# Kernel tuning notes

Measured on AMD Instinct MI355X. Metric: run time of the kernel, lower is better.

Reference implementation:

```python
import jax, jax.numpy as jnp
import numpy as np

LORA_ALPHA = 32
RANK = 16
TOP_K = 2
SCALING = LORA_ALPHA / RANK  # lora_alpha / r
EPS = 1e-9


def setup_inputs() -> dict:
    key = jax.random.key(0)
    ks = jax.random.split(key, 6)
    B, S, D_IN, D_OUT, E, R = 4, 2048, 4096, 4096, 8, RANK
    x = jax.random.normal(ks[0], (B, S, D_IN), dtype=jnp.float32)
    W = jax.random.normal(ks[1], (D_OUT, D_IN), dtype=jnp.float32) * (1.0 / np.sqrt(D_IN))
    bias = jax.random.normal(ks[2], (D_OUT,), dtype=jnp.float32) * 0.02
    route_W = jax.random.normal(ks[3], (E, D_IN), dtype=jnp.float32) * (1.0 / np.sqrt(D_IN))
    lora_A = jax.random.normal(ks[4], (E, R, D_IN), dtype=jnp.float32) * (1.0 / np.sqrt(D_IN))
    lora_B = jax.random.normal(ks[5], (D_OUT, R), dtype=jnp.float32)
    lora_B = jnp.broadcast_to(lora_B, (E, D_OUT, R)) * 0.01  # small nonzero so lora path matters
    return {"x": x, "W": W, "bias": bias, "route_W": route_W,
            "lora_A": lora_A, "lora_B": jnp.asarray(lora_B)}


def reference(x, W, bias, route_W, lora_A, lora_B):
    # Base dense projection: y = x W^T + b   [B,S,out]
    base = jnp.einsum('bsi,oi->bso', x, W) + bias

    # Router: softmax over experts in fp32, then top-k gating
    gate_score = jnp.einsum('bsi,ei->bse', x, route_W)          # [B,S,E]
    probs = jax.nn.softmax(gate_score.astype(jnp.float32), axis=-1)
    topk_vals, topk_idx = jax.lax.top_k(probs, TOP_K)           # [B,S,k]
    # renorm (top_k < lora_nums)
    topk_vals = topk_vals / (jnp.sum(topk_vals, axis=-1, keepdims=True) + EPS)
    # dense routing weights: zeros with top-k values scattered back  [B,S,E]
    E = probs.shape[-1]
    routing_weight = jnp.sum(
        jax.nn.one_hot(topk_idx, E, dtype=base.dtype) * topk_vals[..., None].astype(base.dtype),
        axis=-2)

    # Expert LoRA: identical math to the gather/index_add loop, expressed as
    # a dense weighted combine (weights are exactly 0 for unrouted experts).
    xf = x.astype(jnp.float32)
    h = jnp.einsum('bsi,eri->bser', xf, lora_A.astype(jnp.float32))      # [B,S,E,r] (small)
    hw = h * routing_weight.astype(jnp.float32)[..., None]               # gate per expert
    lora_out = jnp.einsum('bser,eor->bso', hw, lora_B.astype(jnp.float32))

    result = base + lora_out.astype(base.dtype) * SCALING
    return result, routing_weight, gate_score
```

## Files before the change

### kernel.cpp

```cpp
#include <hip/hip_runtime.h>
#include <hip/hip_bf16.h>

typedef __bf16 bf16_t;
typedef __bf16 bf16x8 __attribute__((ext_vector_type(8)));
typedef float floatx4 __attribute__((ext_vector_type(4)));

#define M_TOK 8192
#define K_DIM 4096
#define N_OUT 4096
#define NEXP  8
#define LRANK 16
#define KEXT  128
#define SCALING 2.0f

#define GLOAD_LDS16(g, l) \
    __builtin_amdgcn_global_load_lds((const __attribute__((address_space(1))) void*)(g), \
                                     (__attribute__((address_space(3))) void*)(l), 16, 0, 0)


__device__ __forceinline__ void pack4(bf16_t* dst, float4 v) {
    union { bf16_t h[4]; uint2 u; } t;
    t.h[0] = (bf16_t)v.x; t.h[1] = (bf16_t)v.y;
    t.h[2] = (bf16_t)v.z; t.h[3] = (bf16_t)v.w;
    *(uint2*)dst = t.u;
}

__device__ __forceinline__ void cvt8_body(const float* __restrict__ src,
                                          bf16_t* __restrict__ dst, int blk) {
    size_t i = (size_t)blk * 256 + threadIdx.x;
    float4 a = ((const float4*)src)[i * 2];
    float4 b = ((const float4*)src)[i * 2 + 1];
    union { bf16_t h[8]; uint4 u; } t;
    t.h[0] = (bf16_t)a.x; t.h[1] = (bf16_t)a.y; t.h[2] = (bf16_t)a.z; t.h[3] = (bf16_t)a.w;
    t.h[4] = (bf16_t)b.x; t.h[5] = (bf16_t)b.y; t.h[6] = (bf16_t)b.z; t.h[7] = (bf16_t)b.w;
    ((uint4*)dst)[i] = t.u;
}


#define PREP_W_BLKS   8192
#define PREP_A_BLKS   256
#define PREP_B_BLKS   2048

__global__ __launch_bounds__(256) void prep_all(const float* __restrict__ W,
                                                const float* __restrict__ loraA,
                                                const float* __restrict__ loraB,
                                                bf16_t* __restrict__ Wb,
                                                bf16_t* __restrict__ aflat,
                                                bf16_t* __restrict__ bflat) {
    int b = blockIdx.x;
    if (b < PREP_W_BLKS) {
        cvt8_body(W, Wb, b);
    } else if (b < PREP_W_BLKS + PREP_A_BLKS) {
        cvt8_body(loraA, aflat, b - PREP_W_BLKS);
    } else {
        int g = (b - PREP_W_BLKS - PREP_A_BLKS) * 256 + threadIdx.x;
        int o = g >> 7, j = g & 127;
        int e = j >> 4, r = j & 15;
        bflat[g] = (bf16_t)loraB[((size_t)e * N_OUT + o) * LRANK + r];
    }
}


__global__ __launch_bounds__(256) void gate_cvt16(const float* __restrict__ x,
                                                  const float* __restrict__ routeW,
                                                  bf16_t* __restrict__ xb,
                                                  float* __restrict__ rw_out,
                                                  float* __restrict__ gate_out)
{
    __shared__ float rwT[NEXP][256];
    int tid = threadIdx.x, lane = tid & 63, wave = tid >> 6;
    int tl = lane >> 4, seg = lane & 15;
    int t = blockIdx.x * 16 + wave * 4 + tl;
    const float* xrow = x + (size_t)t * K_DIM;
    bf16_t* xbrow = xb + (size_t)t * K_DIM;

    float acc[NEXP];
    #pragma unroll
    for (int e = 0; e < NEXP; ++e) acc[e] = 0.f;

    int srow = tid >> 5, scol = (tid & 31) * 8;

    for (int kk = 0; kk < K_DIM / 256; ++kk) {
        {
            const float4* src = (const float4*)(routeW + (size_t)srow * K_DIM + kk * 256 + scol);
            float4 v0 = src[0], v1 = src[1];
            *(float4*)&rwT[srow][scol]     = v0;
            *(float4*)&rwT[srow][scol + 4] = v1;
        }
        __syncthreads();
        #pragma unroll
        for (int kc = 0; kc < 4; ++kc) {
            int kloc = kc * 64 + seg * 4;
            int k = kk * 256 + kloc;
            float4 xv = *(const float4*)(xrow + k);
            union { bf16_t h[4]; uint2 u; } cv;
            cv.h[0] = (bf16_t)xv.x; cv.h[1] = (bf16_t)xv.y;
            cv.h[2] = (bf16_t)xv.z; cv.h[3] = (bf16_t)xv.w;
            *(uint2*)(xbrow + k) = cv.u;
            #pragma unroll
            for (int e = 0; e < NEXP; ++e) {
                float4 wv = *(const float4*)&rwT[e][kloc];
                acc[e] += xv.x * wv.x + xv.y * wv.y + xv.z * wv.z + xv.w * wv.w;
            }
        }
        __syncthreads();
    }

    #pragma unroll
    for (int e = 0; e < NEXP; ++e) {
        acc[e] += __shfl_xor(acc[e], 1);
        acc[e] += __shfl_xor(acc[e], 2);
        acc[e] += __shfl_xor(acc[e], 4);
        acc[e] += __shfl_xor(acc[e], 8);
    }

    if (seg == 0) {
        float mx = acc[0];
        #pragma unroll
        for (int e = 1; e < NEXP; ++e) mx = fmaxf(mx, acc[e]);
        float p[NEXP], s = 0.f;
        #pragma unroll
        for (int e = 0; e < NEXP; ++e) { p[e] = expf(acc[e] - mx); s += p[e]; }
        float inv_s = 1.0f / s;
        #pragma unroll
        for (int e = 0; e < NEXP; ++e) p[e] *= inv_s;
        int i0 = 0;
        #pragma unroll
        for (int e = 1; e < NEXP; ++e) if (p[e] > p[i0]) i0 = e;
        int i1 = (i0 == 0) ? 1 : 0;
        #pragma unroll
        for (int e = 0; e < NEXP; ++e) { if (e == i0 || e == i1) continue; if (p[e] > p[i1]) i1 = e; }
        float v0 = p[i0], v1 = p[i1];
        float inv = 1.0f / (v0 + v1 + 1e-9f);
        float r[NEXP];
        #pragma unroll
        for (int e = 0; e < NEXP; ++e) r[e] = 0.f;
        r[i0] = v0 * inv; r[i1] = v1 * inv;
        #pragma unroll
        for (int e = 0; e < NEXP; ++e) {
            gate_out[(size_t)t * NEXP + e] = acc[e];
            rw_out[(size_t)t * NEXP + e]  = r[e];
        }
    }
}


__global__ __launch_bounds__(256) void h_kernel_v3(const bf16_t* __restrict__ xb,
                                                   const bf16_t* __restrict__ aflat,
                                                   const float* __restrict__ rw,
                                                   bf16_t* __restrict__ hw)
{
    __shared__ bf16_t As[4 * 32 * 32];
    __shared__ bf16_t Bs[4 * 128 * 32];
    int tid = threadIdx.x, lane = tid & 63, wave = tid >> 6;
    int lrow = lane & 15, lq = lane >> 4;
    int n0 = wave * 32;
    int m0 = blockIdx.x * 32;
    floatx4 acc[2][2] = {};

    const bf16_t* srcA[2];
    #pragma unroll
    for (int i = 0; i < 2; ++i) {
        int idx = i * 256 + tid;
        int ks = idx >> 7, r = (idx >> 2) & 31, cc2 = idx & 3;
        srcA[i] = xb + (size_t)(m0 + r) * K_DIM + ks * 32 + cc2 * 8;
    }
    const bf16_t* srcB[8];
    #pragma unroll
    for (int i = 0; i < 8; ++i) {
        int idx = i * 256 + tid;
        int ks = idx >> 9, r = (idx >> 2) & 127, cc2 = idx & 3;
        srcB[i] = aflat + (size_t)r * K_DIM + ks * 32 + cc2 * 8;
    }

    for (int k0 = 0; k0 < K_DIM; k0 += 128) {
        #pragma unroll
        for (int i = 0; i < 2; ++i)
            GLOAD_LDS16(srcA[i] + k0, (char*)As + (i * 256 + wave * 64) * 16);
        #pragma unroll
        for (int i = 0; i < 8; ++i)
            GLOAD_LDS16(srcB[i] + k0, (char*)Bs + (i * 256 + wave * 64) * 16);
        __syncthreads();
        #pragma unroll
        for (int ks = 0; ks < 4; ++ks) {
            bf16x8 af[2], bfr[2];
            #pragma unroll
            for (int mi = 0; mi < 2; ++mi)
                af[mi] = *(const bf16x8*)(As + ks * 1024 + (mi * 16 + lrow) * 32 + lq * 8);
            #pragma unroll
            for (int ni = 0; ni < 2; ++ni)
                bfr[ni] = *(const bf16x8*)(Bs + ks * 4096 + (n0 + ni * 16 + lrow) * 32 + lq * 8);
            #pragma unroll
            for (int mi = 0; mi < 2; ++mi)
                #pragma unroll
                for (int ni = 0; ni < 2; ++ni)
                    acc[mi][ni] = __builtin_amdgcn_mfma_f32_16x16x32_bf16(af[mi], bfr[ni], acc[mi][ni], 0, 0, 0);
        }
        __syncthreads();
    }
    #pragma unroll
    for (int mi = 0; mi < 2; ++mi)
        #pragma unroll
        for (int ni = 0; ni < 2; ++ni)
            #pragma unroll
            for (int reg = 0; reg < 4; ++reg) {
                int t = m0 + mi * 16 + lq * 4 + reg;
                int j = n0 + ni * 16 + lrow;
                float g = rw[(size_t)t * NEXP + (j >> 4)] * SCALING;
                hw[(size_t)t * KEXT + j] = (bf16_t)(acc[mi][ni][reg] * g);
            }
}


__global__ __launch_bounds__(256) void main_gemm_fast(const bf16_t* __restrict__ xb,
                                                      const bf16_t* __restrict__ Wb,
                                                      const float* __restrict__ bias,
                                                      const bf16_t* __restrict__ hw,
                                                      const bf16_t* __restrict__ bflat,
                                                      float* __restrict__ out)
{
    __shared__ bf16_t As[128 * 32];
    __shared__ bf16_t Bs[128 * 32];
    int tid = threadIdx.x, lane = tid & 63, wave = tid >> 6;
    int lrow = lane & 15, lq = lane >> 4;
    int wm = (wave >> 1) * 64, wn = (wave & 1) * 64;
    int tm = blockIdx.y * 128, tn = blockIdx.x * 128;
    floatx4 acc[4][4] = {};

    int r0 = tid >> 2;
    int cg = (tid & 3) * 8;
    const bf16_t* gA0 = xb + (size_t)(tm + r0) * K_DIM + cg;
    const bf16_t* gA1 = xb + (size_t)(tm + 64 + r0) * K_DIM + cg;
    const bf16_t* gB0 = Wb + (size_t)(tn + r0) * K_DIM + cg;
    const bf16_t* gB1 = Wb + (size_t)(tn + 64 + r0) * K_DIM + cg;
    bf16_t* lA0 = As + wave * 512;
    bf16_t* lA1 = As + 2048 + wave * 512;
    bf16_t* lB0 = Bs + wave * 512;
    bf16_t* lB1 = Bs + 2048 + wave * 512;

    for (int k0 = 0; k0 < K_DIM; k0 += 32) {
        GLOAD_LDS16(gA0 + k0, lA0);
        GLOAD_LDS16(gA1 + k0, lA1);
        GLOAD_LDS16(gB0 + k0, lB0);
        GLOAD_LDS16(gB1 + k0, lB1);
        __syncthreads();
        bf16x8 af[4], bfr[4];
        #pragma unroll
        for (int mi = 0; mi < 4; ++mi) af[mi] = *(const bf16x8*)(As + (wm + mi * 16 + lrow) * 32 + lq * 8);
        #pragma unroll
        for (int ni = 0; ni < 4; ++ni) bfr[ni] = *(const bf16x8*)(Bs + (wn + ni * 16 + lrow) * 32 + lq * 8);
        #pragma unroll
        for (int mi = 0; mi < 4; ++mi)
            #pragma unroll
            for (int ni = 0; ni < 4; ++ni)
                acc[mi][ni] = __builtin_amdgcn_mfma_f32_16x16x32_bf16(af[mi], bfr[ni], acc[mi][ni], 0, 0, 0);
        __syncthreads();
    }

    {
        const bf16_t* eA0 = hw    + (size_t)(tm + r0) * KEXT + cg;
        const bf16_t* eA1 = hw    + (size_t)(tm + 64 + r0) * KEXT + cg;
        const bf16_t* eB0 = bflat + (size_t)(tn + r0) * KEXT + cg;
        const bf16_t* eB1 = bflat + (size_t)(tn + 64 + r0) * KEXT + cg;
        for (int k0 = 0; k0 < KEXT; k0 += 32) {
            GLOAD_LDS16(eA0 + k0, lA0);
            GLOAD_LDS16(eA1 + k0, lA1);
            GLOAD_LDS16(eB0 + k0, lB0);
            GLOAD_LDS16(eB1 + k0, lB1);
            __syncthreads();
            bf16x8 af[4], bfr[4];
            #pragma unroll
            for (int mi = 0; mi < 4; ++mi) af[mi] = *(const bf16x8*)(As + (wm + mi * 16 + lrow) * 32 + lq * 8);
            #pragma unroll
            for (int ni = 0; ni < 4; ++ni) bfr[ni] = *(const bf16x8*)(Bs + (wn + ni * 16 + lrow) * 32 + lq * 8);
            #pragma unroll
            for (int mi = 0; mi < 4; ++mi)
                #pragma unroll
                for (int ni = 0; ni < 4; ++ni)
                    acc[mi][ni] = __builtin_amdgcn_mfma_f32_16x16x32_bf16(af[mi], bfr[ni], acc[mi][ni], 0, 0, 0);
            __syncthreads();
        }
    }

    #pragma unroll
    for (int mi = 0; mi < 4; ++mi)
        #pragma unroll
        for (int ni = 0; ni < 4; ++ni) {
            int row = tm + wm + mi * 16 + lq * 4;
            int col = tn + wn + ni * 16 + lrow;
            float b = bias[col];
            #pragma unroll
            for (int reg = 0; reg < 4; ++reg)
                out[(size_t)(row + reg) * N_OUT + col] = acc[mi][ni][reg] + b;
        }
}


__global__ __launch_bounds__(256) void prep_bflat(const float* __restrict__ loraB,
                                                  bf16_t* __restrict__ bflat) {
    int g = blockIdx.x * 256 + threadIdx.x;
    int o = g >> 7, j = g & 127;
    int e = j >> 4, r = j & 15;
    bflat[g] = (bf16_t)loraB[((size_t)e * N_OUT + o) * LRANK + r];
}

__global__ __launch_bounds__(256) void gate_kernel(const float* __restrict__ x,
                                                   const float* __restrict__ routeW,
                                                   float* __restrict__ rw_out,
                                                   float* __restrict__ gate_out)
{
    int wave = threadIdx.x >> 6;
    int lane = threadIdx.x & 63;
    int t = blockIdx.x * 4 + wave;
    const float4* xp = (const float4*)(x + (size_t)t * K_DIM);
    float acc[NEXP];
    #pragma unroll
    for (int e = 0; e < NEXP; ++e) acc[e] = 0.f;
    #pragma unroll 4
    for (int it = 0; it < K_DIM / 256; ++it) {
        float4 xv = xp[it * 64 + lane];
        #pragma unroll
        for (int e = 0; e < NEXP; ++e) {
            float4 wv = ((const float4*)(routeW + (size_t)e * K_DIM))[it * 64 + lane];
            acc[e] += xv.x * wv.x + xv.y * wv.y + xv.z * wv.z + xv.w * wv.w;
        }
    }
    #pragma unroll
    for (int e = 0; e < NEXP; ++e)
        for (int off = 32; off > 0; off >>= 1)
            acc[e] += __shfl_xor(acc[e], off, 64);
    if (lane == 0) {
        float mx = acc[0];
        #pragma unroll
        for (int e = 1; e < NEXP; ++e) mx = fmaxf(mx, acc[e]);
        float p[NEXP], s = 0.f;
        #pragma unroll
        for (int e = 0; e < NEXP; ++e) { p[e] = expf(acc[e] - mx); s += p[e]; }
        float inv_s = 1.0f / s;
        #pragma unroll
        for (int e = 0; e < NEXP; ++e) p[e] *= inv_s;
        int i0 = 0;
        #pragma unroll
        for (int e = 1; e < NEXP; ++e) if (p[e] > p[i0]) i0 = e;
        int i1 = (i0 == 0) ? 1 : 0;
        #pragma unroll
        for (int e = 0; e < NEXP; ++e) { if (e == i0 || e == i1) continue; if (p[e] > p[i1]) i1 = e; }
        float v0 = p[i0], v1 = p[i1];
        float inv = 1.0f / (v0 + v1 + 1e-9f);
        float r[NEXP];
        #pragma unroll
        for (int e = 0; e < NEXP; ++e) r[e] = 0.f;
        r[i0] = v0 * inv; r[i1] = v1 * inv;
        #pragma unroll
        for (int e = 0; e < NEXP; ++e) {
            gate_out[(size_t)t * NEXP + e] = acc[e];
            rw_out[(size_t)t * NEXP + e]  = r[e];
        }
    }
}

__global__ __launch_bounds__(256) void h_kernel(const float* __restrict__ x,
                                                const float* __restrict__ loraA,
                                                const float* __restrict__ rw,
                                                bf16_t* __restrict__ hw)
{
    __shared__ bf16_t As[32][40];
    __shared__ bf16_t Bs[128][40];
    int tid = threadIdx.x;
    int wave = tid >> 6, lane = tid & 63;
    int lrow = lane & 15, lq = lane >> 4;
    int m0 = blockIdx.x * 32;
    floatx4 acc[2][2] = {};
    int rb = tid >> 1, cb = (tid & 1) * 16;
    for (int k0 = 0; k0 < K_DIM; k0 += 32) {
        if (tid < 64) {
            const float* srcA = x + (size_t)(m0 + rb) * K_DIM + k0 + cb;
            #pragma unroll
            for (int q = 0; q < 4; ++q) pack4(&As[rb][cb + q * 4], ((const float4*)srcA)[q]);
        }
        {
            const float* srcB = loraA + (size_t)rb * K_DIM + k0 + cb;
            #pragma unroll
            for (int q = 0; q < 4; ++q) pack4(&Bs[rb][cb + q * 4], ((const float4*)srcB)[q]);
        }
        __syncthreads();
        bf16x8 af[2], bfr[2];
        #pragma unroll
        for (int mi = 0; mi < 2; ++mi) af[mi] = *(const bf16x8*)&As[mi * 16 + lrow][lq * 8];
        #pragma unroll
        for (int ni = 0; ni < 2; ++ni) bfr[ni] = *(const bf16x8*)&Bs[wave * 32 + ni * 16 + lrow][lq * 8];
        #pragma unroll
        for (int mi = 0; mi < 2; ++mi)
            #pragma unroll
            for (int ni = 0; ni < 2; ++ni)
                acc[mi][ni] = __builtin_amdgcn_mfma_f32_16x16x32_bf16(af[mi], bfr[ni], acc[mi][ni], 0, 0, 0);
        __syncthreads();
    }
    #pragma unroll
    for (int mi = 0; mi < 2; ++mi)
        #pragma unroll
        for (int ni = 0; ni < 2; ++ni)
            #pragma unroll
            for (int reg = 0; reg < 4; ++reg) {
                int t = m0 + mi * 16 + lq * 4 + reg;
                int j = wave * 32 + ni * 16 + lrow;
                float g = rw[(size_t)t * NEXP + (j >> 4)] * SCALING;
                hw[(size_t)t * KEXT + j] = (bf16_t)(acc[mi][ni][reg] * g);
            }
}

__device__ __forceinline__ void mma_step(const bf16_t (*As)[40], const bf16_t (*Bs)[40],
                                         floatx4 acc[4][4], int wm, int wn, int lrow, int lq) {
    bf16x8 af[4], bfr[4];
    #pragma unroll
    for (int mi = 0; mi < 4; ++mi) af[mi] = *(const bf16x8*)&As[wm + mi * 16 + lrow][lq * 8];
    #pragma unroll
    for (int ni = 0; ni < 4; ++ni) bfr[ni] = *(const bf16x8*)&Bs[wn + ni * 16 + lrow][lq * 8];
    #pragma unroll
    for (int mi = 0; mi < 4; ++mi)
        #pragma unroll
        for (int ni = 0; ni < 4; ++ni)
            acc[mi][ni] = __builtin_amdgcn_mfma_f32_16x16x32_bf16(af[mi], bfr[ni], acc[mi][ni], 0, 0, 0);
}

__global__ __launch_bounds__(256) void main_gemm(const float* __restrict__ x,
                                                 const float* __restrict__ W,
                                                 const float* __restrict__ bias,
                                                 const bf16_t* __restrict__ hw,
                                                 const bf16_t* __restrict__ bflat,
                                                 float* __restrict__ out)
{
    __shared__ bf16_t As[128][40];
    __shared__ bf16_t Bs[128][40];
    int tid = threadIdx.x, lane = tid & 63, wave = tid >> 6;
    int lrow = lane & 15, lq = lane >> 4;
    int wm = (wave >> 1) * 64, wn = (wave & 1) * 64;
    int tm = blockIdx.y * 128, tn = blockIdx.x * 128;
    floatx4 acc[4][4] = {};
    int rb = tid >> 1, cb = (tid & 1) * 16;
    const float* gA = x + (size_t)(tm + rb) * K_DIM + cb;
    const float* gB = W + (size_t)(tn + rb) * K_DIM + cb;
    for (int k0 = 0; k0 < K_DIM; k0 += 32) {
        #pragma unroll
        for (int q = 0; q < 4; ++q) {
            pack4(&As[rb][cb + q * 4], ((const float4*)(gA + k0))[q]);
            pack4(&Bs[rb][cb + q * 4], ((const float4*)(gB + k0))[q]);
        }
        __syncthreads();
        mma_step(As, Bs, acc, wm, wn, lrow, lq);
        __syncthreads();
    }
    const bf16_t* eA = hw    + (size_t)(tm + rb) * KEXT + cb;
    const bf16_t* eB = bflat + (size_t)(tn + rb) * KEXT + cb;
    for (int k0 = 0; k0 < KEXT; k0 += 32) {
        *(uint4*)&As[rb][cb]     = *(const uint4*)(eA + k0);
        *(uint4*)&As[rb][cb + 8] = *(const uint4*)(eA + k0 + 8);
        *(uint4*)&Bs[rb][cb]     = *(const uint4*)(eB + k0);
        *(uint4*)&Bs[rb][cb + 8] = *(const uint4*)(eB + k0 + 8);
        __syncthreads();
        mma_step(As, Bs, acc, wm, wn, lrow, lq);
        __syncthreads();
    }
    #pragma unroll
    for (int mi = 0; mi < 4; ++mi)
        #pragma unroll
        for (int ni = 0; ni < 4; ++ni) {
            int row = tm + wm + mi * 16 + lq * 4;
            int col = tn + wn + ni * 16 + lrow;
            float b = bias[col];
            #pragma unroll
            for (int reg = 0; reg < 4; ++reg)
                out[(size_t)(row + reg) * N_OUT + col] = acc[mi][ni][reg] + b;
        }
}


extern "C" void kernel_launch(void* const* d_in, const int* in_sizes, int n_in,
                              void* d_out, int out_size, void* d_ws, size_t ws_size,
                              hipStream_t stream) {
    const float* x      = (const float*)d_in[0];
    const float* W      = (const float*)d_in[1];
    const float* bias   = (const float*)d_in[2];
    const float* routeW = (const float*)d_in[3];
    const float* loraA  = (const float*)d_in[4];
    const float* loraB  = (const float*)d_in[5];

    float* out0 = (float*)d_out;
    float* out1 = out0 + (size_t)M_TOK * N_OUT;
    float* out2 = out1 + (size_t)M_TOK * NEXP;

    size_t need = ((size_t)M_TOK * K_DIM + (size_t)N_OUT * K_DIM +
                   (size_t)KEXT * K_DIM + (size_t)N_OUT * KEXT +
                   (size_t)M_TOK * KEXT) * sizeof(bf16_t);

    if (ws_size >= need) {
        bf16_t* xb    = (bf16_t*)d_ws;
        bf16_t* Wb    = xb + (size_t)M_TOK * K_DIM;
        bf16_t* aflat = Wb + (size_t)N_OUT * K_DIM;
        bf16_t* bflat = aflat + (size_t)KEXT * K_DIM;
        bf16_t* hw    = bflat + (size_t)N_OUT * KEXT;

        hipLaunchKernelGGL(prep_all, dim3(PREP_W_BLKS + PREP_A_BLKS + PREP_B_BLKS), dim3(256), 0, stream,
                           W, loraA, loraB, Wb, aflat, bflat);
        hipLaunchKernelGGL(gate_cvt16, dim3(M_TOK / 16), dim3(256), 0, stream, x, routeW, xb, out1, out2);
        hipLaunchKernelGGL(h_kernel_v3, dim3(M_TOK / 32), dim3(256), 0, stream, xb, aflat, out1, hw);
        hipLaunchKernelGGL(main_gemm_fast, dim3(N_OUT / 128, M_TOK / 128), dim3(256), 0, stream,
                           xb, Wb, bias, hw, bflat, out0);
    } else {
        bf16_t* bflat = (bf16_t*)d_ws;
        bf16_t* hw    = bflat + (size_t)N_OUT * KEXT;
        hipLaunchKernelGGL(prep_bflat, dim3((N_OUT * KEXT) / 256), dim3(256), 0, stream, loraB, bflat);
        hipLaunchKernelGGL(gate_kernel, dim3(M_TOK / 4), dim3(256), 0, stream, x, routeW, out1, out2);
        hipLaunchKernelGGL(h_kernel, dim3(M_TOK / 32), dim3(256), 0, stream, x, loraA, out1, hw);
        hipLaunchKernelGGL(main_gemm, dim3(N_OUT / 128, M_TOK / 128), dim3(256), 0, stream,
                           x, W, bias, hw, bflat, out0);
    }
}
```

Measured before the change: 695.0 us.

## Double K-tile depth to 64 and XOR-swizzle LDS layout in main GEMM

The main GEMM now stages 64-wide K slices per iteration instead of 32, halving the number of barrier pairs per tile. LDS columns are XOR-swizzled by row so the 128-byte row stride no longer causes bank conflicts on the MFMA fragment reads. This doubles LDS use per block to 32 KB, which could limit occupancy, but needs no extra registers.

After: 605.8 us. 1.15x faster.

```diff
diff --git a/kernel.cpp b/kernel.cpp
--- a/kernel.cpp
+++ b/kernel.cpp
@@ -212,72 +212,94 @@
 }
 
 
-__global__ __launch_bounds__(256) void main_gemm_fast(const bf16_t* __restrict__ xb,
-                                                      const bf16_t* __restrict__ Wb,
-                                                      const float* __restrict__ bias,
-                                                      const bf16_t* __restrict__ hw,
-                                                      const bf16_t* __restrict__ bflat,
-                                                      float* __restrict__ out)
+__global__ __launch_bounds__(256) void main_gemm_v2(const bf16_t* __restrict__ xb,
+                                                    const bf16_t* __restrict__ Wb,
+                                                    const float* __restrict__ bias,
+                                                    const bf16_t* __restrict__ hw,
+                                                    const bf16_t* __restrict__ bflat,
+                                                    float* __restrict__ out)
 {
-    __shared__ bf16_t As[128 * 32];
-    __shared__ bf16_t Bs[128 * 32];
+    __shared__ bf16_t As[128 * 64];
+    __shared__ bf16_t Bs[128 * 64];
     int tid = threadIdx.x, lane = tid & 63, wave = tid >> 6;
     int lrow = lane & 15, lq = lane >> 4;
     int wm = (wave >> 1) * 64, wn = (wave & 1) * 64;
     int tm = blockIdx.y * 128, tn = blockIdx.x * 128;
     floatx4 acc[4][4] = {};
 
-    int r0 = tid >> 2;
-    int cg = (tid & 3) * 8;
-    const bf16_t* gA0 = xb + (size_t)(tm + r0) * K_DIM + cg;
-    const bf16_t* gA1 = xb + (size_t)(tm + 64 + r0) * K_DIM + cg;
-    const bf16_t* gB0 = Wb + (size_t)(tn + r0) * K_DIM + cg;
-    const bf16_t* gB1 = Wb + (size_t)(tn + 64 + r0) * K_DIM + cg;
-    bf16_t* lA0 = As + wave * 512;
-    bf16_t* lA1 = As + 2048 + wave * 512;
-    bf16_t* lB0 = Bs + wave * 512;
-    bf16_t* lB1 = Bs + 2048 + wave * 512;
-
-    for (int k0 = 0; k0 < K_DIM; k0 += 32) {
-        GLOAD_LDS16(gA0 + k0, lA0);
-        GLOAD_LDS16(gA1 + k0, lA1);
-        GLOAD_LDS16(gB0 + k0, lB0);
-        GLOAD_LDS16(gB1 + k0, lB1);
-        __syncthreads();
-        bf16x8 af[4], bfr[4];
-        #pragma unroll
-        for (int mi = 0; mi < 4; ++mi) af[mi] = *(const bf16x8*)(As + (wm + mi * 16 + lrow) * 32 + lq * 8);
-        #pragma unroll
-        for (int ni = 0; ni < 4; ++ni) bfr[ni] = *(const bf16x8*)(Bs + (wn + ni * 16 + lrow) * 32 + lq * 8);
-        #pragma unroll
-        for (int mi = 0; mi < 4; ++mi)
+    const bf16_t* srcA[4];
+    const bf16_t* srcB[4];
+    #pragma unroll
+    for (int i = 0; i < 4; ++i) {
+        int s = i * 256 + tid;
+        int row = s >> 3;
+        int lg = (s & 7) ^ (row & 7);
+        srcA[i] = xb + (size_t)(tm + row) * K_DIM + lg * 8;
+        srcB[i] = Wb + (size_t)(tn + row) * K_DIM + lg * 8;
+    }
+
+    int swz = lrow & 7;
+
+    for (int k0 = 0; k0 < K_DIM; k0 += 64) {
+        #pragma unroll
+        for (int i = 0; i < 4; ++i) {
+            GLOAD_LDS16(srcA[i] + k0, (char*)As + i * 4096 + wave * 1024);
+            GLOAD_LDS16(srcB[i] + k0, (char*)Bs + i * 4096 + wave * 1024);
+        }
+        __syncthreads();
+        #pragma unroll
+        for (int ks = 0; ks < 2; ++ks) {
+            int go = ((ks * 4 + lq) ^ swz) * 8;
+            bf16x8 af[4], bfr[4];
+            #pragma unroll
+            for (int mi = 0; mi < 4; ++mi)
+                af[mi] = *(const bf16x8*)(As + (wm + mi * 16 + lrow) * 64 + go);
             #pragma unroll
             for (int ni = 0; ni < 4; ++ni)
-                acc[mi][ni] = __builtin_amdgcn_mfma_f32_16x16x32_bf16(af[mi], bfr[ni], acc[mi][ni], 0, 0, 0);
-        __syncthreads();
-    }
-
-    {
-        const bf16_t* eA0 = hw    + (size_t)(tm + r0) * KEXT + cg;
-        const bf16_t* eA1 = hw    + (size_t)(tm + 64 + r0) * KEXT + cg;
-        const bf16_t* eB0 = bflat + (size_t)(tn + r0) * KEXT + cg;
-        const bf16_t* eB1 = bflat + (size_t)(tn + 64 + r0) * KEXT + cg;
-        for (int k0 = 0; k0 < KEXT; k0 += 32) {
-            GLOAD_LDS16(eA0 + k0, lA0);
-            GLOAD_LDS16(eA1 + k0, lA1);
-            GLOAD_LDS16(eB0 + k0, lB0);
-            GLOAD_LDS16(eB1 + k0, lB1);
-            __syncthreads();
-            bf16x8 af[4], bfr[4];
-            #pragma unroll
-            for (int mi = 0; mi < 4; ++mi) af[mi] = *(const bf16x8*)(As + (wm + mi * 16 + lrow) * 32 + lq * 8);
-            #pragma unroll
-            for (int ni = 0; ni < 4; ++ni) bfr[ni] = *(const bf16x8*)(Bs + (wn + ni * 16 + lrow) * 32 + lq * 8);
+                bfr[ni] = *(const bf16x8*)(Bs + (wn + ni * 16 + lrow) * 64 + go);
             #pragma unroll
             for (int mi = 0; mi < 4; ++mi)
                 #pragma unroll
                 for (int ni = 0; ni < 4; ++ni)
                     acc[mi][ni] = __builtin_amdgcn_mfma_f32_16x16x32_bf16(af[mi], bfr[ni], acc[mi][ni], 0, 0, 0);
+        }
+        __syncthreads();
+    }
+
+    {
+        const bf16_t* eA[4];
+        const bf16_t* eB[4];
+        #pragma unroll
+        for (int i = 0; i < 4; ++i) {
+            int s = i * 256 + tid;
+            int row = s >> 3;
+            int lg = (s & 7) ^ (row & 7);
+            eA[i] = hw    + (size_t)(tm + row) * KEXT + lg * 8;
+            eB[i] = bflat + (size_t)(tn + row) * KEXT + lg * 8;
+        }
+        for (int k0 = 0; k0 < KEXT; k0 += 64) {
+            #pragma unroll
+            for (int i = 0; i < 4; ++i) {
+                GLOAD_LDS16(eA[i] + k0, (char*)As + i * 4096 + wave * 1024);
+                GLOAD_LDS16(eB[i] + k0, (char*)Bs + i * 4096 + wave * 1024);
+            }
+            __syncthreads();
+            #pragma unroll
+            for (int ks = 0; ks < 2; ++ks) {
+                int go = ((ks * 4 + lq) ^ swz) * 8;
+                bf16x8 af[4], bfr[4];
+                #pragma unroll
+                for (int mi = 0; mi < 4; ++mi)
+                    af[mi] = *(const bf16x8*)(As + (wm + mi * 16 + lrow) * 64 + go);
+                #pragma unroll
+                for (int ni = 0; ni < 4; ++ni)
+                    bfr[ni] = *(const bf16x8*)(Bs + (wn + ni * 16 + lrow) * 64 + go);
+                #pragma unroll
+                for (int mi = 0; mi < 4; ++mi)
+                    #pragma unroll
+                    for (int ni = 0; ni < 4; ++ni)
+                        acc[mi][ni] = __builtin_amdgcn_mfma_f32_16x16x32_bf16(af[mi], bfr[ni], acc[mi][ni], 0, 0, 0);
+            }
             __syncthreads();
         }
     }
@@ -504,7 +526,7 @@
                            W, loraA, loraB, Wb, aflat, bflat);
         hipLaunchKernelGGL(gate_cvt16, dim3(M_TOK / 16), dim3(256), 0, stream, x, routeW, xb, out1, out2);
         hipLaunchKernelGGL(h_kernel_v3, dim3(M_TOK / 32), dim3(256), 0, stream, xb, aflat, out1, hw);
-        hipLaunchKernelGGL(main_gemm_fast, dim3(N_OUT / 128, M_TOK / 128), dim3(256), 0, stream,
+        hipLaunchKernelGGL(main_gemm_v2, dim3(N_OUT / 128, M_TOK / 128), dim3(256), 0, stream,
                            xb, Wb, bias, hw, bflat, out0);
     } else {
         bf16_t* bflat = (bf16_t*)d_ws;
```
